# Optimization experiments

Measured on AMD Instinct MI355X. Metric: run time of the kernel, lower is better.

Reference implementation:

```python
import jax, jax.numpy as jnp
import numpy as np

B, T, IN_DIM = 128, 4096, 13
UNITS, MOTOR = 64, 6
LAYERS = [35, 23, 6]   # AutoNCP(64, 6): inter / command / motor neurons
_SPLITS = [35, 58]     # cumulative layer boundaries inside the 64-unit state


def setup_inputs() -> dict:
    keys = iter(jax.random.split(jax.random.key(0), 64))
    def rn(shape, s=0.1):
        return jax.random.normal(next(keys), shape, dtype=jnp.float32) * s
    inp = {"x": jax.random.normal(next(keys), (B, T, IN_DIM), dtype=jnp.float32)}
    # mixed-memory LSTM cell (ncps: input_map has bias, recurrent_map does not)
    inp["lstm_wi"] = rn((4 * UNITS, IN_DIM))
    inp["lstm_wh"] = rn((4 * UNITS, UNITS))
    inp["lstm_b"] = rn((4 * UNITS,))
    # wired CfC layers: ff1/ff2/time_a/time_b acting on concat([input, h])
    in_dims = [IN_DIM] + LAYERS[:-1]
    for i, (d, h) in enumerate(zip(in_dims, LAYERS)):
        for nm in ("w1", "w2", "wa", "wb"):
            inp[f"cfc{i}_{nm}"] = rn((h, d + h))
        for nm in ("b1", "b2", "ba", "bb"):
            inp[f"cfc{i}_{nm}"] = rn((h,))
    inp["gyro_w1"] = rn((32, MOTOR)); inp["gyro_b1"] = rn((32,))
    inp["gyro_w2"] = rn((3, 32));     inp["gyro_b2"] = rn((3,))
    inp["acc_w1"] = rn((32, MOTOR));  inp["acc_b1"] = rn((32,))
    inp["acc_w2"] = rn((3, 32));      inp["acc_b2"] = rn((3,))
    inp["unc_w1"] = rn((16, MOTOR));  inp["unc_b1"] = rn((16,))
    inp["unc_w2"] = rn((6, 16));      inp["unc_b2"] = rn((6,))
    return inp


def _cfc_step(inp, h, p):
    """ncps CfCCell, mode='default', no backbone, ts = 1.0."""
    W1, b1, W2, b2, Wa, ba, Wb, bb = p
    z = jnp.concatenate([inp, h], axis=-1)            # (B, in+hid)
    ff1 = jnp.tanh(z @ W1.T + b1)
    ff2 = jnp.tanh(z @ W2.T + b2)
    t = jax.nn.sigmoid((z @ Wa.T + ba) + (z @ Wb.T + bb))  # t_a*ts + t_b, ts==1
    return ff1 * (1.0 - t) + t * ff2


def reference(x, lstm_wi, lstm_wh, lstm_b,
              cfc0_w1, cfc0_b1, cfc0_w2, cfc0_b2, cfc0_wa, cfc0_ba, cfc0_wb, cfc0_bb,
              cfc1_w1, cfc1_b1, cfc1_w2, cfc1_b2, cfc1_wa, cfc1_ba, cfc1_wb, cfc1_bb,
              cfc2_w1, cfc2_b1, cfc2_w2, cfc2_b2, cfc2_wa, cfc2_ba, cfc2_wb, cfc2_bb,
              gyro_w1, gyro_b1, gyro_w2, gyro_b2,
              acc_w1, acc_b1, acc_w2, acc_b2,
              unc_w1, unc_b1, unc_w2, unc_b2):
    layer_params = (
        (cfc0_w1, cfc0_b1, cfc0_w2, cfc0_b2, cfc0_wa, cfc0_ba, cfc0_wb, cfc0_bb),
        (cfc1_w1, cfc1_b1, cfc1_w2, cfc1_b2, cfc1_wa, cfc1_ba, cfc1_wb, cfc1_bb),
        (cfc2_w1, cfc2_b1, cfc2_w2, cfc2_b2, cfc2_wa, cfc2_ba, cfc2_wb, cfc2_bb),
    )

    def step(carry, xt):  # xt: (B, 13)
        h, c = carry
        # mixed-memory LSTM over the full 64-unit state (forget gate +1.0)
        zg = xt @ lstm_wi.T + lstm_b + h @ lstm_wh.T
        ia, ig, fg, og = jnp.split(zg, 4, axis=-1)
        c_new = c * jax.nn.sigmoid(fg + 1.0) + jnp.tanh(ia) * jax.nn.sigmoid(ig)
        h_lstm = jnp.tanh(c_new) * jax.nn.sigmoid(og)
        # wired CfC: inter -> command -> motor, each fed previous layer's output
        hs = jnp.split(h_lstm, _SPLITS, axis=-1)
        inp = xt
        new_hs = []
        for hi, p in zip(hs, layer_params):
            inp = _cfc_step(inp, hi, p)
            new_hs.append(inp)
        return (jnp.concatenate(new_hs, axis=-1), c_new), inp  # motor out (B,6)

    Bsz = x.shape[0]
    h0 = jnp.zeros((Bsz, UNITS), x.dtype)
    c0 = jnp.zeros((Bsz, UNITS), x.dtype)
    _, outs = jax.lax.scan(step, (h0, c0), jnp.swapaxes(x, 0, 1))
    cfc_out = jnp.swapaxes(outs, 0, 1)  # (B, T, 6)

    gyro = jnp.tanh(cfc_out @ gyro_w1.T + gyro_b1) @ gyro_w2.T + gyro_b2
    acc = jnp.tanh(cfc_out @ acc_w1.T + acc_b1) @ acc_w2.T + acc_b2
    pred = jnp.concatenate([gyro, acc], axis=-1)                      # (B, T, 6)
    unc = jax.nn.softplus(
        jax.nn.relu(cfc_out @ unc_w1.T + unc_b1) @ unc_w2.T + unc_b2)  # (B, T, 6)
    return pred, unc
```

## Files before the change

### kernel.cpp

```cpp
#include <hip/hip_runtime.h>
#include <math.h>

#define BATCH 128
#define TSTEPS 4096
#define INDIM 13
#define XT 64


__device__ __forceinline__ float fsig(float x) {
    return __builtin_amdgcn_rcpf(1.f + __expf(-x));
}
__device__ __forceinline__ float ftanh(float x) {
    float s = fsig(x + x);
    return s + s - 1.f;
}
__device__ __forceinline__ float fsoftplus(float x) {
    return (x > 15.f) ? x : __logf(1.f + __expf(x));
}

__device__ __forceinline__ float qxor1(float v) {
    return __int_as_float(__builtin_amdgcn_update_dpp(
        0, __float_as_int(v), 0xB1, 0xF, 0xF, true));
}
__device__ __forceinline__ float qxor2(float v) {
    return __int_as_float(__builtin_amdgcn_update_dpp(
        0, __float_as_int(v), 0x4E, 0xF, 0xF, true));
}
#define BFLY4(a) { a += qxor1(a); a += qxor2(a); }

#define FMA4(acc, W, q, zv) { acc += zv.x * W##_##q##_0; acc += zv.y * W##_##q##_1; \
                              acc += zv.z * W##_##q##_2; acc += zv.w * W##_##q##_3; }

__global__ __launch_bounds__(256, 1)
void rnn_kernel(const float* __restrict__ x,
                const float* __restrict__ lstm_wi, const float* __restrict__ lstm_wh,
                const float* __restrict__ lstm_b,
                const float* __restrict__ c0w1, const float* __restrict__ c0w2,
                const float* __restrict__ c0wa, const float* __restrict__ c0wb,
                const float* __restrict__ c0b1, const float* __restrict__ c0b2,
                const float* __restrict__ c0ba, const float* __restrict__ c0bb,
                const float* __restrict__ c1w1, const float* __restrict__ c1w2,
                const float* __restrict__ c1wa, const float* __restrict__ c1wb,
                const float* __restrict__ c1b1, const float* __restrict__ c1b2,
                const float* __restrict__ c1ba, const float* __restrict__ c1bb,
                const float* __restrict__ c2w1, const float* __restrict__ c2w2,
                const float* __restrict__ c2wa, const float* __restrict__ c2wb,
                const float* __restrict__ c2b1, const float* __restrict__ c2b2,
                const float* __restrict__ c2ba, const float* __restrict__ c2bb,
                float* __restrict__ out)
{
    const int bb = blockIdx.x;
    const int t  = threadIdx.x;
    const int k  = t & 3;
    const int u  = t >> 2;

    __shared__ __align__(16) float smem[2688];
    float* zL  = smem;
    float* z0  = smem + 96;
    float* z1  = smem + 160;
    float* z2  = smem + 224;
    float* xt0 = smem + 256;
    float* xt1 = smem + 1088;
    float* ot0 = smem + 1920;
    float* ot1 = smem + 2304;

    const long xbase = (long)bb * TSTEPS * INDIM;
    const long obase = (long)bb * TSTEPS * 6;

    auto lwf = [&](int A, int c) -> float {
        int r = A * 64 + u;
        return (c < 13) ? lstm_wi[r * 13 + c]
             : (c < 77) ? lstm_wh[r * 64 + (c - 13)] : 0.f;
    };
#define DEF_WL(A,q) \
    float wl##A##_##q##_0 = lwf(A, 24*k + 4*q + 0); \
    float wl##A##_##q##_1 = lwf(A, 24*k + 4*q + 1); \
    float wl##A##_##q##_2 = lwf(A, 24*k + 4*q + 2); \
    float wl##A##_##q##_3 = lwf(A, 24*k + 4*q + 3);
    DEF_WL(0,0) DEF_WL(0,1) DEF_WL(0,2) DEF_WL(0,3) DEF_WL(0,4) DEF_WL(0,5)
    DEF_WL(1,0) DEF_WL(1,1) DEF_WL(1,2) DEF_WL(1,3) DEF_WL(1,4) DEF_WL(1,5)
    DEF_WL(2,0) DEF_WL(2,1) DEF_WL(2,2) DEF_WL(2,3) DEF_WL(2,4) DEF_WL(2,5)
    DEF_WL(3,0) DEF_WL(3,1) DEF_WL(3,2) DEF_WL(3,3) DEF_WL(3,4) DEF_WL(3,5)
#undef DEF_WL
    const float bL0 = lstm_b[u];
    const float bL1 = lstm_b[64 + u];
    const float bL2 = lstm_b[128 + u];
    const float bL3 = lstm_b[192 + u];

    const int grp  = (u < 35) ? 0 : (u < 58) ? 1 : 2;
    const int row  = (grp == 0) ? u : (grp == 1) ? (u - 35) : (u - 58);
    const int rl   = (grp == 0) ? 48 : (grp == 1) ? 58 : 29;
    const int clen = (grp == 0) ? 12 : (grp == 1) ? 16 : 8;
    const int cb   = clen * k;
    const float *W0p, *W1p, *W2p, *W3p;
    float bC0, bC1, bC2, bC3;
    if (grp == 0) {
        W0p = c0w1 + row * 48; W1p = c0w2 + row * 48;
        W2p = c0wa + row * 48; W3p = c0wb + row * 48;
        bC0 = c0b1[row]; bC1 = c0b2[row]; bC2 = c0ba[row]; bC3 = c0bb[row];
    } else if (grp == 1) {
        W0p = c1w1 + row * 58; W1p = c1w2 + row * 58;
        W2p = c1wa + row * 58; W3p = c1wb + row * 58;
        bC0 = c1b1[row]; bC1 = c1b2[row]; bC2 = c1ba[row]; bC3 = c1bb[row];
    } else {
        W0p = c2w1 + row * 29; W1p = c2w2 + row * 29;
        W2p = c2wa + row * 29; W3p = c2wb + row * 29;
        bC0 = c2b1[row]; bC1 = c2b2[row]; bC2 = c2ba[row]; bC3 = c2bb[row];
    }
    auto cwf = [&](const float* W, int c) -> float {
        int cc = cb + c;
        return (c < clen && cc < rl) ? W[cc] : 0.f;
    };
#define DEF_WC(A,q) \
    float wc##A##_##q##_0 = cwf(W##A##p, 4*q + 0); \
    float wc##A##_##q##_1 = cwf(W##A##p, 4*q + 1); \
    float wc##A##_##q##_2 = cwf(W##A##p, 4*q + 2); \
    float wc##A##_##q##_3 = cwf(W##A##p, 4*q + 3);
    DEF_WC(0,0) DEF_WC(0,1) DEF_WC(0,2) DEF_WC(0,3)
    DEF_WC(1,0) DEF_WC(1,1) DEF_WC(1,2) DEF_WC(1,3)
    DEF_WC(2,0) DEF_WC(2,1) DEF_WC(2,2) DEF_WC(2,3)
    DEF_WC(3,0) DEF_WC(3,1) DEF_WC(3,2) DEF_WC(3,3)
#undef DEF_WC

    float creg = 0.f;

    smem[t] = 0.f;
    if (t < 208) {
        float4 xi = *(const float4*)(x + xbase + 4 * t);
        *(float4*)&xt0[4 * t] = xi;
    }
    if (t < 13) { float x0 = x[xbase + t]; zL[t] = x0; z0[t] = x0; }
    __syncthreads();

    #pragma unroll 1
    for (int ts = 0; ts < TSTEPS; ++ts) {
        const int par = (ts >> 6) & 1;
        const int lts = ts & 63;

        {
            const float4* zc = (const float4*)(zL + 24 * k);
            float4 q0 = zc[0], q1 = zc[1], q2 = zc[2],
                   q3 = zc[3], q4 = zc[4], q5 = zc[5];
            float a0 = 0.f, a1 = 0.f, a2 = 0.f, a3 = 0.f;
            FMA4(a0, wl0, 0, q0) FMA4(a0, wl0, 1, q1) FMA4(a0, wl0, 2, q2)
            FMA4(a0, wl0, 3, q3) FMA4(a0, wl0, 4, q4) FMA4(a0, wl0, 5, q5)
            FMA4(a1, wl1, 0, q0) FMA4(a1, wl1, 1, q1) FMA4(a1, wl1, 2, q2)
            FMA4(a1, wl1, 3, q3) FMA4(a1, wl1, 4, q4) FMA4(a1, wl1, 5, q5)
            FMA4(a2, wl2, 0, q0) FMA4(a2, wl2, 1, q1) FMA4(a2, wl2, 2, q2)
            FMA4(a2, wl2, 3, q3) FMA4(a2, wl2, 4, q4) FMA4(a2, wl2, 5, q5)
            FMA4(a3, wl3, 0, q0) FMA4(a3, wl3, 1, q1) FMA4(a3, wl3, 2, q2)
            FMA4(a3, wl3, 3, q3) FMA4(a3, wl3, 4, q4) FMA4(a3, wl3, 5, q5)
            BFLY4(a0) BFLY4(a1) BFLY4(a2) BFLY4(a3)
            a0 += bL0; a1 += bL1; a2 += bL2; a3 += bL3;
            float cn = creg * fsig(a2 + 1.f) + ftanh(a0) * fsig(a1);
            creg = cn;
            float hl = ftanh(cn) * fsig(a3);
            if (k == 0) {
                if (u < 35)      z0[13 + u] = hl;
                else if (u < 58) z1[u]      = hl;
                else             z2[u - 35] = hl;
            }
        }
        __syncthreads();

        if (grp == 0) {
            const float4* zc = (const float4*)(z0 + 12 * k);
            float4 v0 = zc[0], v1 = zc[1], v2 = zc[2];
            float a0 = 0.f, a1 = 0.f, a2 = 0.f, a3 = 0.f;
            FMA4(a0, wc0, 0, v0) FMA4(a0, wc0, 1, v1) FMA4(a0, wc0, 2, v2)
            FMA4(a1, wc1, 0, v0) FMA4(a1, wc1, 1, v1) FMA4(a1, wc1, 2, v2)
            FMA4(a2, wc2, 0, v0) FMA4(a2, wc2, 1, v1) FMA4(a2, wc2, 2, v2)
            FMA4(a3, wc3, 0, v0) FMA4(a3, wc3, 1, v1) FMA4(a3, wc3, 2, v2)
            BFLY4(a0) BFLY4(a1) BFLY4(a2) BFLY4(a3)
            a0 += bC0; a1 += bC1; a2 += bC2; a3 += bC3;
            float tg = fsig(a2 + a3);
            float f1 = ftanh(a0), f2 = ftanh(a1);
            float o = f1 + tg * (f2 - f1);
            if (k == 0) { z1[row] = o; zL[13 + row] = o; }
        } else {
            if (lts == 62 && (ts + 2) < TSTEPS) {
                int i = (t - 140) * 2;
                float* dst = par ? xt0 : xt1;
                const float* src = x + xbase + (long)(ts + 2) * 13;
                if (i < 208)     *(float4*)&dst[4*i]     = *(const float4*)(src + 4*i);
                if (i + 1 < 208) *(float4*)&dst[4*(i+1)] = *(const float4*)(src + 4*(i+1));
            }
            if (lts == 0 && ts > 0) {
                int i = t - 140;
                if (i < 96) {
                    const float* src = par ? ot0 : ot1;
                    float4 v = *(const float4*)&src[4 * i];
                    *(float4*)(out + obase + (long)(ts - XT) * 6 + 4 * i) = v;
                }
            }
        }
        __syncthreads();

        if (grp == 1) {
            const float4* zc = (const float4*)(z1 + 16 * k);
            float4 v0 = zc[0], v1 = zc[1], v2 = zc[2], v3 = zc[3];
            float a0 = 0.f, a1 = 0.f, a2 = 0.f, a3 = 0.f;
            FMA4(a0, wc0, 0, v0) FMA4(a0, wc0, 1, v1) FMA4(a0, wc0, 2, v2) FMA4(a0, wc0, 3, v3)
            FMA4(a1, wc1, 0, v0) FMA4(a1, wc1, 1, v1) FMA4(a1, wc1, 2, v2) FMA4(a1, wc1, 3, v3)
            FMA4(a2, wc2, 0, v0) FMA4(a2, wc2, 1, v1) FMA4(a2, wc2, 2, v2) FMA4(a2, wc2, 3, v3)
            FMA4(a3, wc3, 0, v0) FMA4(a3, wc3, 1, v1) FMA4(a3, wc3, 2, v2) FMA4(a3, wc3, 3, v3)
            BFLY4(a0) BFLY4(a1) BFLY4(a2) BFLY4(a3)
            a0 += bC0; a1 += bC1; a2 += bC2; a3 += bC3;
            float tg = fsig(a2 + a3);
            float f1 = ftanh(a0), f2 = ftanh(a1);
            float o = f1 + tg * (f2 - f1);
            if (k == 0) { z2[row] = o; zL[48 + row] = o; }
        }
        __syncthreads();

        if (grp == 2) {
            const float4* zc = (const float4*)(z2 + 8 * k);
            float4 v0 = zc[0], v1 = zc[1];
            float a0 = 0.f, a1 = 0.f, a2 = 0.f, a3 = 0.f;
            FMA4(a0, wc0, 0, v0) FMA4(a0, wc0, 1, v1)
            FMA4(a1, wc1, 0, v0) FMA4(a1, wc1, 1, v1)
            FMA4(a2, wc2, 0, v0) FMA4(a2, wc2, 1, v1)
            FMA4(a3, wc3, 0, v0) FMA4(a3, wc3, 1, v1)
            BFLY4(a0) BFLY4(a1) BFLY4(a2) BFLY4(a3)
            a0 += bC0; a1 += bC1; a2 += bC2; a3 += bC3;
            float tg = fsig(a2 + a3);
            float f1 = ftanh(a0), f2 = ftanh(a1);
            float o = f1 + tg * (f2 - f1);
            if (k == 0) {
                zL[71 + row] = o;
                float* ob = par ? ot1 : ot0;
                ob[lts * 6 + row] = o;
            }
        } else if (t < 13 && (ts + 1) < TSTEPS) {
            const float* xb = (((ts + 1) >> 6) & 1) ? xt1 : xt0;
            float xn = xb[((ts + 1) & 63) * 13 + t];
            zL[t] = xn; z0[t] = xn;
        }
        __syncthreads();
    }

    if (t < 96) {
        float4 v = *(const float4*)&ot1[4 * t];
        *(float4*)(out + obase + (long)(TSTEPS - XT) * 6 + 4 * t) = v;
    }
}

#define S_GW1 0
#define S_GB1 192
#define S_GW2 224
#define S_GB2 320
#define S_AW1 323
#define S_AB1 515
#define S_AW2 547
#define S_AB2 643
#define S_UW1 646
#define S_UB1 742
#define S_UW2 758
#define S_UB2 854
#define S_TOT 860

__global__ __launch_bounds__(256)
void head_kernel(const float* __restrict__ gw1, const float* __restrict__ gb1,
                 const float* __restrict__ gw2, const float* __restrict__ gb2,
                 const float* __restrict__ aw1, const float* __restrict__ ab1,
                 const float* __restrict__ aw2, const float* __restrict__ ab2,
                 const float* __restrict__ uw1, const float* __restrict__ ub1,
                 const float* __restrict__ uw2, const float* __restrict__ ub2,
                 float* __restrict__ out)
{
    __shared__ float s[S_TOT];
    const int t = threadIdx.x;
    if (t < 192) { s[S_GW1 + t] = gw1[t]; s[S_AW1 + t] = aw1[t]; }
    if (t < 96)  { s[S_GW2 + t] = gw2[t]; s[S_AW2 + t] = aw2[t];
                   s[S_UW1 + t] = uw1[t]; s[S_UW2 + t] = uw2[t]; }
    if (t < 32)  { s[S_GB1 + t] = gb1[t]; s[S_AB1 + t] = ab1[t]; }
    if (t < 16)  { s[S_UB1 + t] = ub1[t]; }
    if (t < 3)   { s[S_GB2 + t] = gb2[t]; s[S_AB2 + t] = ab2[t]; }
    if (t < 6)   { s[S_UB2 + t] = ub2[t]; }
    __syncthreads();

    const long p = (long)blockIdx.x * 256 + t;
    const long base = p * 6;
    float m0 = out[base+0], m1 = out[base+1], m2 = out[base+2];
    float m3 = out[base+3], m4 = out[base+4], m5 = out[base+5];

    float gy0 = s[S_GB2+0], gy1 = s[S_GB2+1], gy2 = s[S_GB2+2];
    float ac0 = s[S_AB2+0], ac1 = s[S_AB2+1], ac2 = s[S_AB2+2];
    #pragma unroll
    for (int i = 0; i < 32; ++i) {
        float hg = s[S_GB1+i] + s[S_GW1+i*6+0]*m0 + s[S_GW1+i*6+1]*m1
                 + s[S_GW1+i*6+2]*m2 + s[S_GW1+i*6+3]*m3
                 + s[S_GW1+i*6+4]*m4 + s[S_GW1+i*6+5]*m5;
        hg = ftanh(hg);
// ... 80 lines not shown
```

Baseline: 5.327 ms.

## Restructure recurrent step into two barriers with per-wave redundant CfC layers

Reorganizes each timestep so the command and motor CfC layers are computed redundantly inside every wavefront, using wave-local LDS copies and an lgkmcnt fence in place of block-wide barriers, then fuses them with the next LSTM step. The inter layer and the input staging run in a first phase. State buffers are double-buffered by timestep parity, and the loop gains a prologue iteration. This cuts the per-step __syncthreads from four to two, which shortens the serial critical path. The cost is extra redundant compute, more registers for the duplicated weights, and reliance on the LDS fence giving correct intra-wave ordering.

```diff
diff --git a/kernel.cpp b/kernel.cpp
--- a/kernel.cpp
+++ b/kernel.cpp
@@ -30,6 +30,9 @@
 
 #define FMA4(acc, W, q, zv) { acc += zv.x * W##_##q##_0; acc += zv.y * W##_##q##_1; \
                               acc += zv.z * W##_##q##_2; acc += zv.w * W##_##q##_3; }
+
+#define LDS_FENCE() { asm volatile("s_waitcnt lgkmcnt(0)" ::: "memory"); \
+                      __builtin_amdgcn_sched_barrier(0); }
 
 __global__ __launch_bounds__(256, 1)
 void rnn_kernel(const float* __restrict__ x,
@@ -53,16 +56,22 @@
     const int t  = threadIdx.x;
     const int k  = t & 3;
     const int u  = t >> 2;
-
-    __shared__ __align__(16) float smem[2688];
-    float* zL  = smem;
-    float* z0  = smem + 96;
-    float* z1  = smem + 160;
-    float* z2  = smem + 224;
-    float* xt0 = smem + 256;
-    float* xt1 = smem + 1088;
-    float* ot0 = smem + 1920;
-    float* ot1 = smem + 2304;
+    const int l  = t & 63;
+    const int w  = t >> 6;
+    const int cu1 = l >> 1, h1 = l & 1;
+    const int c2i = l - 46;
+    const int cu2 = c2i >> 1, h2 = c2i & 1;
+
+    __shared__ __align__(16) float smem[3152];
+    float* z0  = smem;
+    float* zLa = smem + 96;
+    float* z1  = smem + 144;
+    float* z2  = smem + 272;
+    float* zLb = smem + 528;
+    float* xt0 = smem + 720;
+    float* xt1 = smem + 1552;
+    float* ot0 = smem + 2384;
+    float* ot1 = smem + 2768;
 
     const long xbase = (long)bb * TSTEPS * INDIM;
     const long obase = (long)bb * TSTEPS * 6;
@@ -87,154 +96,215 @@
     const float bL2 = lstm_b[128 + u];
     const float bL3 = lstm_b[192 + u];
 
-    const int grp  = (u < 35) ? 0 : (u < 58) ? 1 : 2;
-    const int row  = (grp == 0) ? u : (grp == 1) ? (u - 35) : (u - 58);
-    const int rl   = (grp == 0) ? 48 : (grp == 1) ? 58 : 29;
-    const int clen = (grp == 0) ? 12 : (grp == 1) ? 16 : 8;
-    const int cb   = clen * k;
-    const float *W0p, *W1p, *W2p, *W3p;
-    float bC0, bC1, bC2, bC3;
-    if (grp == 0) {
-        W0p = c0w1 + row * 48; W1p = c0w2 + row * 48;
-        W2p = c0wa + row * 48; W3p = c0wb + row * 48;
-        bC0 = c0b1[row]; bC1 = c0b2[row]; bC2 = c0ba[row]; bC3 = c0bb[row];
-    } else if (grp == 1) {
-        W0p = c1w1 + row * 58; W1p = c1w2 + row * 58;
-        W2p = c1wa + row * 58; W3p = c1wb + row * 58;
-        bC0 = c1b1[row]; bC1 = c1b2[row]; bC2 = c1ba[row]; bC3 = c1bb[row];
-    } else {
-        W0p = c2w1 + row * 29; W1p = c2w2 + row * 29;
-        W2p = c2wa + row * 29; W3p = c2wb + row * 29;
-        bC0 = c2b1[row]; bC1 = c2b2[row]; bC2 = c2ba[row]; bC3 = c2bb[row];
-    }
-    auto cwf = [&](const float* W, int c) -> float {
-        int cc = cb + c;
-        return (c < clen && cc < rl) ? W[cc] : 0.f;
+    const float *P0 = c0w1, *P1 = c0w2, *P2 = c0wa, *P3 = c0wb;
+    auto c0f = [&](const float* Wp, int c) -> float {
+        return (t < 140) ? Wp[u * 48 + 12 * k + c] : 0.f;
     };
-#define DEF_WC(A,q) \
-    float wc##A##_##q##_0 = cwf(W##A##p, 4*q + 0); \
-    float wc##A##_##q##_1 = cwf(W##A##p, 4*q + 1); \
-    float wc##A##_##q##_2 = cwf(W##A##p, 4*q + 2); \
-    float wc##A##_##q##_3 = cwf(W##A##p, 4*q + 3);
-    DEF_WC(0,0) DEF_WC(0,1) DEF_WC(0,2) DEF_WC(0,3)
-    DEF_WC(1,0) DEF_WC(1,1) DEF_WC(1,2) DEF_WC(1,3)
-    DEF_WC(2,0) DEF_WC(2,1) DEF_WC(2,2) DEF_WC(2,3)
-    DEF_WC(3,0) DEF_WC(3,1) DEF_WC(3,2) DEF_WC(3,3)
-#undef DEF_WC
+#define DEF_WA(A,q) \
+    float wa##A##_##q##_0 = c0f(P##A, 4*q + 0); \
+    float wa##A##_##q##_1 = c0f(P##A, 4*q + 1); \
+    float wa##A##_##q##_2 = c0f(P##A, 4*q + 2); \
+    float wa##A##_##q##_3 = c0f(P##A, 4*q + 3);
+    DEF_WA(0,0) DEF_WA(0,1) DEF_WA(0,2)
+    DEF_WA(1,0) DEF_WA(1,1) DEF_WA(1,2)
+    DEF_WA(2,0) DEF_WA(2,1) DEF_WA(2,2)
+    DEF_WA(3,0) DEF_WA(3,1) DEF_WA(3,2)
+#undef DEF_WA
+    const float bA0 = (t < 140) ? c0b1[u] : 0.f;
+    const float bA1 = (t < 140) ? c0b2[u] : 0.f;
+    const float bA2 = (t < 140) ? c0ba[u] : 0.f;
+    const float bA3 = (t < 140) ? c0bb[u] : 0.f;
+
+    const float *D0 = c1w1, *D1 = c1w2, *D2 = c1wa, *D3 = c1wb;
+    auto c1f = [&](const float* Wp, int c) -> float {
+        const int col = 32 * h1 + c;
+        return (l < 46 && col < 58) ? Wp[cu1 * 58 + col] : 0.f;
+    };
+#define DEF_WD(A,q) \
+    float wd##A##_##q##_0 = c1f(D##A, 4*q + 0); \
+    float wd##A##_##q##_1 = c1f(D##A, 4*q + 1); \
+    float wd##A##_##q##_2 = c1f(D##A, 4*q + 2); \
+    float wd##A##_##q##_3 = c1f(D##A, 4*q + 3);
+    DEF_WD(0,0) DEF_WD(0,1) DEF_WD(0,2) DEF_WD(0,3)
+    DEF_WD(0,4) DEF_WD(0,5) DEF_WD(0,6) DEF_WD(0,7)
+    DEF_WD(1,0) DEF_WD(1,1) DEF_WD(1,2) DEF_WD(1,3)
+    DEF_WD(1,4) DEF_WD(1,5) DEF_WD(1,6) DEF_WD(1,7)
+    DEF_WD(2,0) DEF_WD(2,1) DEF_WD(2,2) DEF_WD(2,3)
+    DEF_WD(2,4) DEF_WD(2,5) DEF_WD(2,6) DEF_WD(2,7)
+    DEF_WD(3,0) DEF_WD(3,1) DEF_WD(3,2) DEF_WD(3,3)
+    DEF_WD(3,4) DEF_WD(3,5) DEF_WD(3,6) DEF_WD(3,7)
+#undef DEF_WD
+    const float bD0 = (l < 46) ? c1b1[cu1] : 0.f;
+    const float bD1 = (l < 46) ? c1b2[cu1] : 0.f;
+    const float bD2 = (l < 46) ? c1ba[cu1] : 0.f;
+    const float bD3 = (l < 46) ? c1bb[cu1] : 0.f;
+
+    const float *E0 = c2w1, *E1 = c2w2, *E2 = c2wa, *E3 = c2wb;
+    auto c2f = [&](const float* Wp, int c) -> float {
+        const int col = 16 * h2 + c;
+        return (c2i >= 0 && c2i < 12 && col < 29) ? Wp[cu2 * 29 + col] : 0.f;
+    };
+#define DEF_WE(A,q) \
+    float we##A##_##q##_0 = c2f(E##A, 4*q + 0); \
+    float we##A##_##q##_1 = c2f(E##A, 4*q + 1); \
+    float we##A##_##q##_2 = c2f(E##A, 4*q + 2); \
+    float we##A##_##q##_3 = c2f(E##A, 4*q + 3);
+    DEF_WE(0,0) DEF_WE(0,1) DEF_WE(0,2) DEF_WE(0,3)
+    DEF_WE(1,0) DEF_WE(1,1) DEF_WE(1,2) DEF_WE(1,3)
+    DEF_WE(2,0) DEF_WE(2,1) DEF_WE(2,2) DEF_WE(2,3)
+    DEF_WE(3,0) DEF_WE(3,1) DEF_WE(3,2) DEF_WE(3,3)
+#undef DEF_WE
+    const float bE0 = (c2i >= 0 && c2i < 12) ? c2b1[cu2] : 0.f;
+    const float bE1 = (c2i >= 0 && c2i < 12) ? c2b2[cu2] : 0.f;
+    const float bE2 = (c2i >= 0 && c2i < 12) ? c2ba[cu2] : 0.f;
+    const float bE3 = (c2i >= 0 && c2i < 12) ? c2bb[cu2] : 0.f;
 
     float creg = 0.f;
 
-    smem[t] = 0.f;
+    for (int i = t; i < 720; i += 256) smem[i] = 0.f;
     if (t < 208) {
         float4 xi = *(const float4*)(x + xbase + 4 * t);
         *(float4*)&xt0[4 * t] = xi;
     }
-    if (t < 13) { float x0 = x[xbase + t]; zL[t] = x0; z0[t] = x0; }
     __syncthreads();
 
     #pragma unroll 1
-    for (int ts = 0; ts < TSTEPS; ++ts) {
-        const int par = (ts >> 6) & 1;
-        const int lts = ts & 63;
-
-        {
-            const float4* zc = (const float4*)(zL + 24 * k);
-            float4 q0 = zc[0], q1 = zc[1], q2 = zc[2],
-                   q3 = zc[3], q4 = zc[4], q5 = zc[5];
-            float a0 = 0.f, a1 = 0.f, a2 = 0.f, a3 = 0.f;
-            FMA4(a0, wl0, 0, q0) FMA4(a0, wl0, 1, q1) FMA4(a0, wl0, 2, q2)
-            FMA4(a0, wl0, 3, q3) FMA4(a0, wl0, 4, q4) FMA4(a0, wl0, 5, q5)
-            FMA4(a1, wl1, 0, q0) FMA4(a1, wl1, 1, q1) FMA4(a1, wl1, 2, q2)
-            FMA4(a1, wl1, 3, q3) FMA4(a1, wl1, 4, q4) FMA4(a1, wl1, 5, q5)
-            FMA4(a2, wl2, 0, q0) FMA4(a2, wl2, 1, q1) FMA4(a2, wl2, 2, q2)
-            FMA4(a2, wl2, 3, q3) FMA4(a2, wl2, 4, q4) FMA4(a2, wl2, 5, q5)
-            FMA4(a3, wl3, 0, q0) FMA4(a3, wl3, 1, q1) FMA4(a3, wl3, 2, q2)
-            FMA4(a3, wl3, 3, q3) FMA4(a3, wl3, 4, q4) FMA4(a3, wl3, 5, q5)
-            BFLY4(a0) BFLY4(a1) BFLY4(a2) BFLY4(a3)
-            a0 += bL0; a1 += bL1; a2 += bL2; a3 += bL3;
-            float cn = creg * fsig(a2 + 1.f) + ftanh(a0) * fsig(a1);
-            creg = cn;
-            float hl = ftanh(cn) * fsig(a3);
-            if (k == 0) {
-                if (u < 35)      z0[13 + u] = hl;
-                else if (u < 58) z1[u]      = hl;
-                else             z2[u - 35] = hl;
-            }
-        }
-        __syncthreads();
-
-        if (grp == 0) {
-            const float4* zc = (const float4*)(z0 + 12 * k);
+    for (int ts = -1; ts < TSTEPS; ++ts) {
+        const int par0 = ts & 1;
+        const int par1 = par0 ^ 1;
+        const int lts  = ts & 63;
+        const int tpar = (ts >> 6) & 1;
+        const bool run = (ts >= 0);
+
+        if (run && t < 140) {
+            const float4* zc = (const float4*)(z0 + 48 * par0 + 12 * k);
             float4 v0 = zc[0], v1 = zc[1], v2 = zc[2];
             float a0 = 0.f, a1 = 0.f, a2 = 0.f, a3 = 0.f;
-            FMA4(a0, wc0, 0, v0) FMA4(a0, wc0, 1, v1) FMA4(a0, wc0, 2, v2)
-            FMA4(a1, wc1, 0, v0) FMA4(a1, wc1, 1, v1) FMA4(a1, wc1, 2, v2)
-            FMA4(a2, wc2, 0, v0) FMA4(a2, wc2, 1, v1) FMA4(a2, wc2, 2, v2)
-            FMA4(a3, wc3, 0, v0) FMA4(a3, wc3, 1, v1) FMA4(a3, wc3, 2, v2)
+            FMA4(a0, wa0, 0, v0) FMA4(a0, wa0, 1, v1) FMA4(a0, wa0, 2, v2)
+            FMA4(a1, wa1, 0, v0) FMA4(a1, wa1, 1, v1) FMA4(a1, wa1, 2, v2)
+            FMA4(a2, wa2, 0, v0) FMA4(a2, wa2, 1, v1) FMA4(a2, wa2, 2, v2)
+            FMA4(a3, wa3, 0, v0) FMA4(a3, wa3, 1, v1) FMA4(a3, wa3, 2, v2)
             BFLY4(a0) BFLY4(a1) BFLY4(a2) BFLY4(a3)
-            a0 += bC0; a1 += bC1; a2 += bC2; a3 += bC3;
+            a0 += bA0; a1 += bA1; a2 += bA2; a3 += bA3;
             float tg = fsig(a2 + a3);
             float f1 = ftanh(a0), f2 = ftanh(a1);
             float o = f1 + tg * (f2 - f1);
-            if (k == 0) { z1[row] = o; zL[13 + row] = o; }
-        } else {
-            if (lts == 62 && (ts + 2) < TSTEPS) {
+            if (k == 0) { zLa[13 + u] = o; z1[64 * par0 + u] = o; }
+        } else if (t >= 140) {
+            if (run && lts == 62 && (ts + 2) < TSTEPS) {
                 int i = (t - 140) * 2;
-                float* dst = par ? xt0 : xt1;
+                float* dst = tpar ? xt0 : xt1;
                 const float* src = x + xbase + (long)(ts + 2) * 13;
                 if (i < 208)     *(float4*)&dst[4*i]     = *(const float4*)(src + 4*i);
                 if (i + 1 < 208) *(float4*)&dst[4*(i+1)] = *(const float4*)(src + 4*(i+1));
             }
-            if (lts == 0 && ts > 0) {
+            if (run && lts == 0 && ts > 0) {
                 int i = t - 140;
                 if (i < 96) {
-                    const float* src = par ? ot0 : ot1;
+                    const float* src = tpar ? ot0 : ot1;
                     float4 v = *(const float4*)&src[4 * i];
                     *(float4*)(out + obase + (long)(ts - XT) * 6 + 4 * i) = v;
                 }
             }
         }
-        __syncthreads();
-
-        if (grp == 1) {
-            const float4* zc = (const float4*)(z1 + 16 * k);
-            float4 v0 = zc[0], v1 = zc[1], v2 = zc[2], v3 = zc[3];
-            float a0 = 0.f, a1 = 0.f, a2 = 0.f, a3 = 0.f;
-            FMA4(a0, wc0, 0, v0) FMA4(a0, wc0, 1, v1) FMA4(a0, wc0, 2, v2) FMA4(a0, wc0, 3, v3)
-            FMA4(a1, wc1, 0, v0) FMA4(a1, wc1, 1, v1) FMA4(a1, wc1, 2, v2) FMA4(a1, wc1, 3, v3)
-            FMA4(a2, wc2, 0, v0) FMA4(a2, wc2, 1, v1) FMA4(a2, wc2, 2, v2) FMA4(a2, wc2, 3, v3)
-            FMA4(a3, wc3, 0, v0) FMA4(a3, wc3, 1, v1) FMA4(a3, wc3, 2, v2) FMA4(a3, wc3, 3, v3)
-            BFLY4(a0) BFLY4(a1) BFLY4(a2) BFLY4(a3)
-            a0 += bC0; a1 += bC1; a2 += bC2; a3 += bC3;
-            float tg = fsig(a2 + a3);
-            float f1 = ftanh(a0), f2 = ftanh(a1);
-            float o = f1 + tg * (f2 - f1);
-            if (k == 0) { z2[row] = o; zL[48 + row] = o; }
+        if (t >= 140 && t < 166 && (ts + 1) < TSTEPS) {
+            const int i = t - 140;
+            const float* xb = (((ts + 1) >> 6) & 1) ? xt1 : xt0;
+            const int c = (i < 13) ? i : (i - 13);
+            const float xn = xb[((ts + 1) & 63) * 13 + c];
+            if (i < 13) zLa[c] = xn;
+            else        z0[48 * par1 + c] = xn;
         }
         __syncthreads();
 
-        if (grp == 2) {
-            const float4* zc = (const float4*)(z2 + 8 * k);
-            float4 v0 = zc[0], v1 = zc[1];
-            float a0 = 0.f, a1 = 0.f, a2 = 0.f, a3 = 0.f;
-            FMA4(a0, wc0, 0, v0) FMA4(a0, wc0, 1, v1)
-            FMA4(a1, wc1, 0, v0) FMA4(a1, wc1, 1, v1)
-            FMA4(a2, wc2, 0, v0) FMA4(a2, wc2, 1, v1)
-            FMA4(a3, wc3, 0, v0) FMA4(a3, wc3, 1, v1)
-            BFLY4(a0) BFLY4(a1) BFLY4(a2) BFLY4(a3)
-            a0 += bC0; a1 += bC1; a2 += bC2; a3 += bC3;
-            float tg = fsig(a2 + a3);
-            float f1 = ftanh(a0), f2 = ftanh(a1);
-            float o = f1 + tg * (f2 - f1);
-            if (k == 0) {
-                zL[71 + row] = o;
-                float* ob = par ? ot1 : ot0;
-                ob[lts * 6 + row] = o;
-            }
-        } else if (t < 13 && (ts + 1) < TSTEPS) {
-            const float* xb = (((ts + 1) >> 6) & 1) ? xt1 : xt0;
-            float xn = xb[((ts + 1) & 63) * 13 + t];
-            zL[t] = xn; z0[t] = xn;
+        {
+            float4 y0, y1, y2, y3, y4, y5, y6, y7;
+            if (l < 46) {
+                const float4* zc = (const float4*)(z1 + 64 * par0 + 32 * h1);
+                y0 = zc[0]; y1 = zc[1]; y2 = zc[2]; y3 = zc[3];
+                y4 = zc[4]; y5 = zc[5]; y6 = zc[6]; y7 = zc[7];
+            }
+            float4 q0, q1, q2, q3, q4, q5;
+            if (k < 2) {
+                const float4* zc = (const float4*)(zLa + 24 * k);
+                q0 = zc[0]; q1 = zc[1]; q2 = zc[2];
+                q3 = zc[3]; q4 = zc[4]; q5 = zc[5];
+            }
+
+            if (run && l < 46) {
+                float a0 = 0.f, a1 = 0.f, a2 = 0.f, a3 = 0.f;
+                FMA4(a0, wd0, 0, y0) FMA4(a0, wd0, 1, y1) FMA4(a0, wd0, 2, y2) FMA4(a0, wd0, 3, y3)
+                FMA4(a0, wd0, 4, y4) FMA4(a0, wd0, 5, y5) FMA4(a0, wd0, 6, y6) FMA4(a0, wd0, 7, y7)
+                FMA4(a1, wd1, 0, y0) FMA4(a1, wd1, 1, y1) FMA4(a1, wd1, 2, y2) FMA4(a1, wd1, 3, y3)
+                FMA4(a1, wd1, 4, y4) FMA4(a1, wd1, 5, y5) FMA4(a1, wd1, 6, y6) FMA4(a1, wd1, 7, y7)
+                FMA4(a2, wd2, 0, y0) FMA4(a2, wd2, 1, y1) FMA4(a2, wd2, 2, y2) FMA4(a2, wd2, 3, y3)
+                FMA4(a2, wd2, 4, y4) FMA4(a2, wd2, 5, y5) FMA4(a2, wd2, 6, y6) FMA4(a2, wd2, 7, y7)
+                FMA4(a3, wd3, 0, y0) FMA4(a3, wd3, 1, y1) FMA4(a3, wd3, 2, y2) FMA4(a3, wd3, 3, y3)
+                FMA4(a3, wd3, 4, y4) FMA4(a3, wd3, 5, y5) FMA4(a3, wd3, 6, y6) FMA4(a3, wd3, 7, y7)
+                a0 += qxor1(a0); a1 += qxor1(a1); a2 += qxor1(a2); a3 += qxor1(a3);
+                a0 += bD0; a1 += bD1; a2 += bD2; a3 += bD3;
+                float tg = fsig(a2 + a3);
+                float f1 = ftanh(a0), f2 = ftanh(a1);
+                float o = f1 + tg * (f2 - f1);
+                if (h1 == 0) {
+                    z2[64 * w + 32 * par0 + cu1] = o;
+                    zLb[48 * w + cu1] = o;
+                }
+            }
+            LDS_FENCE();
+
+            if (run && c2i >= 0 && c2i < 12) {
+                const float4* zc = (const float4*)(z2 + 64 * w + 32 * par0 + 16 * h2);
+                float4 v0 = zc[0], v1 = zc[1], v2 = zc[2], v3 = zc[3];
+                float a0 = 0.f, a1 = 0.f, a2 = 0.f, a3 = 0.f;
+                FMA4(a0, we0, 0, v0) FMA4(a0, we0, 1, v1) FMA4(a0, we0, 2, v2) FMA4(a0, we0, 3, v3)
+                FMA4(a1, we1, 0, v0) FMA4(a1, we1, 1, v1) FMA4(a1, we1, 2, v2) FMA4(a1, we1, 3, v3)
+                FMA4(a2, we2, 0, v0) FMA4(a2, we2, 1, v1) FMA4(a2, we2, 2, v2) FMA4(a2, we2, 3, v3)
+                FMA4(a3, we3, 0, v0) FMA4(a3, we3, 1, v1) FMA4(a3, we3, 2, v2) FMA4(a3, we3, 3, v3)
+                a0 += qxor1(a0); a1 += qxor1(a1); a2 += qxor1(a2); a3 += qxor1(a3);
+                a0 += bE0; a1 += bE1; a2 += bE2; a3 += bE3;
+                float tg = fsig(a2 + a3);
+                float f1 = ftanh(a0), f2 = ftanh(a1);
+                float o = f1 + tg * (f2 - f1);
+                if (h2 == 0) {
+                    zLb[48 * w + 23 + cu2] = o;
+                    if (w == 0) {
+                        float* ob = tpar ? ot1 : ot0;
+                        ob[lts * 6 + cu2] = o;
+                    }
+                }
+            }
+            LDS_FENCE();
+
+            if (k >= 2) {
+                const float4* zc = (const float4*)(zLb + 48 * w + 24 * (k - 2));
+                q0 = zc[0]; q1 = zc[1]; q2 = zc[2];
+                q3 = zc[3]; q4 = zc[4]; q5 = zc[5];
+            }
+            {
+                float a0 = 0.f, a1 = 0.f, a2 = 0.f, a3 = 0.f;
+                FMA4(a0, wl0, 0, q0) FMA4(a0, wl0, 1, q1) FMA4(a0, wl0, 2, q2)
+                FMA4(a0, wl0, 3, q3) FMA4(a0, wl0, 4, q4) FMA4(a0, wl0, 5, q5)
+                FMA4(a1, wl1, 0, q0) FMA4(a1, wl1, 1, q1) FMA4(a1, wl1, 2, q2)
+                FMA4(a1, wl1, 3, q3) FMA4(a1, wl1, 4, q4) FMA4(a1, wl1, 5, q5)
+                FMA4(a2, wl2, 0, q0) FMA4(a2, wl2, 1, q1) FMA4(a2, wl2, 2, q2)
+                FMA4(a2, wl2, 3, q3) FMA4(a2, wl2, 4, q4) FMA4(a2, wl2, 5, q5)
+                FMA4(a3, wl3, 0, q0) FMA4(a3, wl3, 1, q1) FMA4(a3, wl3, 2, q2)
+                FMA4(a3, wl3, 3, q3) FMA4(a3, wl3, 4, q4) FMA4(a3, wl3, 5, q5)
+                BFLY4(a0) BFLY4(a1) BFLY4(a2) BFLY4(a3)
+                a0 += bL0; a1 += bL1; a2 += bL2; a3 += bL3;
+                float cn = creg * fsig(a2 + 1.f) + ftanh(a0) * fsig(a1);
+                creg = cn;
+                float hl = ftanh(cn) * fsig(a3);
+                if (k == 0) {
+                    if (u < 35)      z0[48 * par1 + 13 + u] = hl;
+                    else if (u < 58) z1[64 * par1 + u]      = hl;
+                    else {
+                        const int j = 32 * par1 + 23 + (u - 58);
+                        z2[j] = hl; z2[64 + j] = hl; z2[128 + j] = hl; z2[192 + j] = hl;
+                    }
+                }
+            }
         }
         __syncthreads();
     }
```

Result: slower. 8.246 ms (+54.8%).

## Fold motor CfC layer into next step's LSTM phase, dropping a barrier

Applied to the files above, without the earlier changes.

Each wavefront now redundantly computes the motor-layer CfC (layer 2) for the previous timestep at the start of the LSTM phase. It uses lanes 40-63 with register-held weights and exchanges the result through per-wave LDS with only an lgkmcnt wait instead of a block barrier. The LSTM then adds the motor contribution explicitly. z0 and the motor hidden slice are double-buffered by step parity, and the x load moves into the layer-0 phase. This removes one of four __syncthreads per timestep, at the cost of extra redundant FMAs and register pressure in every wave plus an epilogue to finish the last step.

```diff
diff --git a/kernel.cpp b/kernel.cpp
--- a/kernel.cpp
+++ b/kernel.cpp
@@ -30,6 +30,9 @@
 
 #define FMA4(acc, W, q, zv) { acc += zv.x * W##_##q##_0; acc += zv.y * W##_##q##_1; \
                               acc += zv.z * W##_##q##_2; acc += zv.w * W##_##q##_3; }
+
+#define LDS_FENCE() { asm volatile("s_waitcnt lgkmcnt(0)" ::: "memory"); \
+                      __builtin_amdgcn_sched_barrier(0); }
 
 __global__ __launch_bounds__(256, 1)
 void rnn_kernel(const float* __restrict__ x,
@@ -53,16 +56,19 @@
     const int t  = threadIdx.x;
     const int k  = t & 3;
     const int u  = t >> 2;
-
-    __shared__ __align__(16) float smem[2688];
+    const int l  = t & 63;
+    const int w  = t >> 6;
+
+    __shared__ __align__(16) float smem[2736];
     float* zL  = smem;
     float* z0  = smem + 96;
-    float* z1  = smem + 160;
-    float* z2  = smem + 224;
-    float* xt0 = smem + 256;
-    float* xt1 = smem + 1088;
-    float* ot0 = smem + 1920;
-    float* ot1 = smem + 2304;
+    float* z1  = smem + 192;
+    float* z2h = smem + 256;
+    float* zLw = smem + 272;
+    float* xt0 = smem + 304;
+    float* xt1 = smem + 1136;
+    float* ot0 = smem + 1968;
+    float* ot1 = smem + 2352;
 
     const long xbase = (long)bb * TSTEPS * INDIM;
     const long obase = (long)bb * TSTEPS * 6;
@@ -122,25 +128,61 @@
     DEF_WC(3,0) DEF_WC(3,1) DEF_WC(3,2) DEF_WC(3,3)
 #undef DEF_WC
 
+    const int c2a = (l >= 40) ? 1 : 0;
+    const int c2k = c2a ? ((l - 40) & 3) : 0;
+    const int c2u = c2a ? ((l - 40) >> 2) : 0;
+    auto gwf = [&](const float* W, int j) -> float {
+        int col = (c2k < 3) ? (8 * c2k + j) : (23 + j);
+        int lim = (c2k < 3) ? 23 : 29;
+        return (c2a && col < lim) ? W[c2u * 29 + col] : 0.f;
+    };
+#define DEF_WG(A,q) \
+    float wg##A##_##q##_0 = gwf(G##A, 4*q + 0); \
+    float wg##A##_##q##_1 = gwf(G##A, 4*q + 1); \
+    float wg##A##_##q##_2 = gwf(G##A, 4*q + 2); \
+    float wg##A##_##q##_3 = gwf(G##A, 4*q + 3);
+    const float *G0 = c2w1, *G1 = c2w2, *G2 = c2wa, *G3 = c2wb;
+    DEF_WG(0,0) DEF_WG(0,1)
+    DEF_WG(1,0) DEF_WG(1,1)
+    DEF_WG(2,0) DEF_WG(2,1)
+    DEF_WG(3,0) DEF_WG(3,1)
+#undef DEF_WG
+    const float bE0 = c2a ? c2b1[c2u] : 0.f;
+    const float bE1 = c2a ? c2b2[c2u] : 0.f;
+    const float bE2 = c2a ? c2ba[c2u] : 0.f;
+    const float bE3 = c2a ? c2bb[c2u] : 0.f;
+
     float creg = 0.f;
 
-    smem[t] = 0.f;
+    for (int i = t; i < 304; i += 256) smem[i] = 0.f;
     if (t < 208) {
         float4 xi = *(const float4*)(x + xbase + 4 * t);
         *(float4*)&xt0[4 * t] = xi;
     }
-    if (t < 13) { float x0 = x[xbase + t]; zL[t] = x0; z0[t] = x0; }
+    if (t < 13) { float x0v = x[xbase + t]; zL[t] = x0v; z0[t] = x0v; }
     __syncthreads();
 
     #pragma unroll 1
     for (int ts = 0; ts < TSTEPS; ++ts) {
-        const int par = (ts >> 6) & 1;
-        const int lts = ts & 63;
+        const int par0 = ts & 1;
+        const int par1 = par0 ^ 1;
+        const int lts  = ts & 63;
+        const int tpar = (ts >> 6) & 1;
 
         {
+            const float* cp = (c2k < 3) ? (zL + 48 + 8 * c2k) : (z2h + 8 * par1);
+            float4 cv0 = ((const float4*)cp)[0];
+            float4 cv1 = ((const float4*)cp)[1];
             const float4* zc = (const float4*)(zL + 24 * k);
             float4 q0 = zc[0], q1 = zc[1], q2 = zc[2],
                    q3 = zc[3], q4 = zc[4], q5 = zc[5];
+
+            float g0 = 0.f, g1 = 0.f, g2 = 0.f, g3 = 0.f;
+            FMA4(g0, wg0, 0, cv0) FMA4(g0, wg0, 1, cv1)
+            FMA4(g1, wg1, 0, cv0) FMA4(g1, wg1, 1, cv1)
+            FMA4(g2, wg2, 0, cv0) FMA4(g2, wg2, 1, cv1)
+            FMA4(g3, wg3, 0, cv0) FMA4(g3, wg3, 1, cv1)
+
             float a0 = 0.f, a1 = 0.f, a2 = 0.f, a3 = 0.f;
             FMA4(a0, wl0, 0, q0) FMA4(a0, wl0, 1, q1) FMA4(a0, wl0, 2, q2)
             FMA4(a0, wl0, 3, q3) FMA4(a0, wl0, 4, q4) FMA4(a0, wl0, 5, q5)
@@ -150,21 +192,51 @@
             FMA4(a2, wl2, 3, q3) FMA4(a2, wl2, 4, q4) FMA4(a2, wl2, 5, q5)
             FMA4(a3, wl3, 0, q0) FMA4(a3, wl3, 1, q1) FMA4(a3, wl3, 2, q2)
             FMA4(a3, wl3, 3, q3) FMA4(a3, wl3, 4, q4) FMA4(a3, wl3, 5, q5)
+
+            BFLY4(g0) BFLY4(g1) BFLY4(g2) BFLY4(g3)
+            g0 += bE0; g1 += bE1; g2 += bE2; g3 += bE3;
+            float tg2 = fsig(g2 + g3);
+            float f1g = ftanh(g0), f2g = ftanh(g1);
+            float og  = f1g + tg2 * (f2g - f1g);
+            if (ts > 0 && c2a && ((l - 40) & 3) == 0) {
+                zLw[8 * w + c2u] = og;
+                if (w == 0) {
+                    float* ob = (((ts - 1) >> 6) & 1) ? ot1 : ot0;
+                    ob[((ts - 1) & 63) * 6 + c2u] = og;
+                }
+            }
+            LDS_FENCE();
+
+            float4 oza = *(const float4*)(zLw + 8 * w);
+            float2 ozb = *(const float2*)(zLw + 8 * w + 4);
+            if (k == 2) {
+                a0 += oza.x * wl0_5_3; a1 += oza.x * wl1_5_3;
+                a2 += oza.x * wl2_5_3; a3 += oza.x * wl3_5_3;
+            } else if (k == 3) {
+                a0 += oza.y * wl0_0_0; a0 += oza.z * wl0_0_1; a0 += oza.w * wl0_0_2;
+                a0 += ozb.x * wl0_0_3; a0 += ozb.y * wl0_1_0;
+                a1 += oza.y * wl1_0_0; a1 += oza.z * wl1_0_1; a1 += oza.w * wl1_0_2;
+                a1 += ozb.x * wl1_0_3; a1 += ozb.y * wl1_1_0;
+                a2 += oza.y * wl2_0_0; a2 += oza.z * wl2_0_1; a2 += oza.w * wl2_0_2;
+                a2 += ozb.x * wl2_0_3; a2 += ozb.y * wl2_1_0;
+                a3 += oza.y * wl3_0_0; a3 += oza.z * wl3_0_1; a3 += oza.w * wl3_0_2;
+                a3 += ozb.x * wl3_0_3; a3 += ozb.y * wl3_1_0;
+            }
             BFLY4(a0) BFLY4(a1) BFLY4(a2) BFLY4(a3)
             a0 += bL0; a1 += bL1; a2 += bL2; a3 += bL3;
             float cn = creg * fsig(a2 + 1.f) + ftanh(a0) * fsig(a1);
             creg = cn;
             float hl = ftanh(cn) * fsig(a3);
             if (k == 0) {
-                if (u < 35)      z0[13 + u] = hl;
-                else if (u < 58) z1[u]      = hl;
-                else             z2[u - 35] = hl;
+                if (u < 35)      z0[48 * par0 + 13 + u] = hl;
+                else if (u < 58) z1[u] = hl;
+                else             z2h[8 * par0 + (u - 58)] = hl;
             }
         }
         __syncthreads();
 
-        if (grp == 0) {
-            const float4* zc = (const float4*)(z0 + 12 * k);
+        if (t < 140) {
+            const float4* zc = (const float4*)(z0 + 48 * par0 + 12 * k);
             float4 v0 = zc[0], v1 = zc[1], v2 = zc[2];
             float a0 = 0.f, a1 = 0.f, a2 = 0.f, a3 = 0.f;
             FMA4(a0, wc0, 0, v0) FMA4(a0, wc0, 1, v1) FMA4(a0, wc0, 2, v2)
@@ -180,7 +252,7 @@
         } else {
             if (lts == 62 && (ts + 2) < TSTEPS) {
                 int i = (t - 140) * 2;
-                float* dst = par ? xt0 : xt1;
+                float* dst = tpar ? xt0 : xt1;
                 const float* src = x + xbase + (long)(ts + 2) * 13;
                 if (i < 208)     *(float4*)&dst[4*i]     = *(const float4*)(src + 4*i);
                 if (i + 1 < 208) *(float4*)&dst[4*(i+1)] = *(const float4*)(src + 4*(i+1));
@@ -188,11 +260,17 @@
             if (lts == 0 && ts > 0) {
                 int i = t - 140;
                 if (i < 96) {
-                    const float* src = par ? ot0 : ot1;
+                    const float* src = tpar ? ot0 : ot1;
                     float4 v = *(const float4*)&src[4 * i];
                     *(float4*)(out + obase + (long)(ts - XT) * 6 + 4 * i) = v;
                 }
             }
+        }
+        if (t >= 192 && t < 205 && (ts + 1) < TSTEPS) {
+            const int i = t - 192;
+            const float* xb = (((ts + 1) >> 6) & 1) ? xt1 : xt0;
+            float xn = xb[((ts + 1) & 63) * 13 + i];
+            zL[i] = xn; z0[48 * par1 + i] = xn;
         }
         __syncthreads();
 
@@ -209,36 +287,29 @@
             float tg = fsig(a2 + a3);
             float f1 = ftanh(a0), f2 = ftanh(a1);
             float o = f1 + tg * (f2 - f1);
-            if (k == 0) { z2[row] = o; zL[48 + row] = o; }
+            if (k == 0) { zL[48 + row] = o; }
         }
         __syncthreads();
-
-        if (grp == 2) {
-            const float4* zc = (const float4*)(z2 + 8 * k);
-            float4 v0 = zc[0], v1 = zc[1];
-            float a0 = 0.f, a1 = 0.f, a2 = 0.f, a3 = 0.f;
-            FMA4(a0, wc0, 0, v0) FMA4(a0, wc0, 1, v1)
-            FMA4(a1, wc1, 0, v0) FMA4(a1, wc1, 1, v1)
-            FMA4(a2, wc2, 0, v0) FMA4(a2, wc2, 1, v1)
-            FMA4(a3, wc3, 0, v0) FMA4(a3, wc3, 1, v1)
-            BFLY4(a0) BFLY4(a1) BFLY4(a2) BFLY4(a3)
-            a0 += bC0; a1 += bC1; a2 += bC2; a3 += bC3;
-            float tg = fsig(a2 + a3);
-            float f1 = ftanh(a0), f2 = ftanh(a1);
-            float o = f1 + tg * (f2 - f1);
-            if (k == 0) {
-                zL[71 + row] = o;
-                float* ob = par ? ot1 : ot0;
-                ob[lts * 6 + row] = o;
-            }
-        } else if (t < 13 && (ts + 1) < TSTEPS) {
-            const float* xb = (((ts + 1) >> 6) & 1) ? xt1 : xt0;
-            float xn = xb[((ts + 1) & 63) * 13 + t];
-            zL[t] = xn; z0[t] = xn;
-        }
-        __syncthreads();
-    }
-
+    }
+
+    {
+        const float* cp = (c2k < 3) ? (zL + 48 + 8 * c2k) : (z2h + 8);
+        float4 cv0 = ((const float4*)cp)[0];
+        float4 cv1 = ((const float4*)cp)[1];
+        float g0 = 0.f, g1 = 0.f, g2 = 0.f, g3 = 0.f;
+        FMA4(g0, wg0, 0, cv0) FMA4(g0, wg0, 1, cv1)
+        FMA4(g1, wg1, 0, cv0) FMA4(g1, wg1, 1, cv1)
+        FMA4(g2, wg2, 0, cv0) FMA4(g2, wg2, 1, cv1)
+        FMA4(g3, wg3, 0, cv0) FMA4(g3, wg3, 1, cv1)
+        BFLY4(g0) BFLY4(g1) BFLY4(g2) BFLY4(g3)
+        g0 += bE0; g1 += bE1; g2 += bE2; g3 += bE3;
+        float tg2 = fsig(g2 + g3);
+        float f1g = ftanh(g0), f2g = ftanh(g1);
+        float og  = f1g + tg2 * (f2g - f1g);
+        if (c2a && ((l - 40) & 3) == 0 && w == 0)
+            ot1[63 * 6 + c2u] = og;
+    }
+    __syncthreads();
     if (t < 96) {
         float4 v = *(const float4*)&ot1[4 * t];
         *(float4*)(out + obase + (long)(TSTEPS - XT) * 6 + 4 * t) = v;
```

Result: slower. 5.598 ms (+5.1%).

## Precompute LSTM input and inter-layer gate partials off the critical path

Applied to the files above, without the earlier changes.

Splits the LSTM gate matvec so the contributions from the next input and the inter-neuron state (which become available early) are computed by idle threads during the command-layer phase and stored in shared memory. The critical LSTM phase then reduces only over the command/motor state (8 columns per lane instead of 24), shortening the serial dependency chain per timestep. In exchange it costs large per-thread weight arrays (98 extra registers on 128 threads), extra shared memory, and a reshuffled zL layout, which may hurt occupancy or cause spills.

```diff
diff --git a/kernel.cpp b/kernel.cpp
--- a/kernel.cpp
+++ b/kernel.cpp
@@ -54,38 +54,55 @@
     const int k  = t & 3;
     const int u  = t >> 2;
 
-    __shared__ __align__(16) float smem[2688];
+    __shared__ __align__(16) float smem[2944];
     float* zL  = smem;
     float* z0  = smem + 96;
     float* z1  = smem + 160;
     float* z2  = smem + 224;
-    float* xt0 = smem + 256;
-    float* xt1 = smem + 1088;
-    float* ot0 = smem + 1920;
-    float* ot1 = smem + 2304;
+    float* Pb  = smem + 256;
+    float* xt0 = smem + 512;
+    float* xt1 = smem + 1344;
+    float* ot0 = smem + 2176;
+    float* ot1 = smem + 2560;
 
     const long xbase = (long)bb * TSTEPS * INDIM;
     const long obase = (long)bb * TSTEPS * 6;
 
-    auto lwf = [&](int A, int c) -> float {
-        int r = A * 64 + u;
-        return (c < 13) ? lstm_wi[r * 13 + c]
-             : (c < 77) ? lstm_wh[r * 64 + (c - 13)] : 0.f;
-    };
-#define DEF_WL(A,q) \
-    float wl##A##_##q##_0 = lwf(A, 24*k + 4*q + 0); \
-    float wl##A##_##q##_1 = lwf(A, 24*k + 4*q + 1); \
-    float wl##A##_##q##_2 = lwf(A, 24*k + 4*q + 2); \
-    float wl##A##_##q##_3 = lwf(A, 24*k + 4*q + 3);
-    DEF_WL(0,0) DEF_WL(0,1) DEF_WL(0,2) DEF_WL(0,3) DEF_WL(0,4) DEF_WL(0,5)
-    DEF_WL(1,0) DEF_WL(1,1) DEF_WL(1,2) DEF_WL(1,3) DEF_WL(1,4) DEF_WL(1,5)
-    DEF_WL(2,0) DEF_WL(2,1) DEF_WL(2,2) DEF_WL(2,3) DEF_WL(2,4) DEF_WL(2,5)
-    DEF_WL(3,0) DEF_WL(3,1) DEF_WL(3,2) DEF_WL(3,3) DEF_WL(3,4) DEF_WL(3,5)
-#undef DEF_WL
+    float wl[4][8];
+    #pragma unroll
+    for (int A = 0; A < 4; ++A) {
+        #pragma unroll
+        for (int j = 0; j < 8; ++j) {
+            const int c = 48 + 8 * k + j;
+            const int r = A * 64 + u;
+            float wv = 0.f;
+            if (c <= 70)                 wv = lstm_wh[r * 64 + (c - 13)];
+            else if (c >= 72 && c <= 77) wv = lstm_wh[r * 64 + (c - 14)];
+            wl[A][j] = wv;
+        }
+    }
     const float bL0 = lstm_b[u];
     const float bL1 = lstm_b[64 + u];
     const float bL2 = lstm_b[128 + u];
     const float bL3 = lstm_b[192 + u];
+
+    float wpx0[13], wpx1[13], wpo0[36], wpo1[36];
+    {
+        const int A  = t & 3;
+        const int u0 = (t >> 2) & 31;
+        const int u1 = 32 + u0;
+        const bool pw = (t < 128);
+        #pragma unroll
+        for (int c = 0; c < 13; ++c) {
+            wpx0[c] = pw ? lstm_wi[(A * 64 + u0) * 13 + c] : 0.f;
+            wpx1[c] = pw ? lstm_wi[(A * 64 + u1) * 13 + c] : 0.f;
+        }
+        #pragma unroll
+        for (int c = 0; c < 36; ++c) {
+            wpo0[c] = (pw && c < 35) ? lstm_wh[(A * 64 + u0) * 64 + c] : 0.f;
+            wpo1[c] = (pw && c < 35) ? lstm_wh[(A * 64 + u1) * 64 + c] : 0.f;
+        }
+    }
 
     const int grp  = (u < 35) ? 0 : (u < 58) ? 1 : 2;
     const int row  = (grp == 0) ? u : (grp == 1) ? (u - 35) : (u - 58);
@@ -124,13 +141,37 @@
 
     float creg = 0.f;
 
-    smem[t] = 0.f;
+    for (int i = t; i < 512; i += 256) smem[i] = 0.f;
     if (t < 208) {
         float4 xi = *(const float4*)(x + xbase + 4 * t);
         *(float4*)&xt0[4 * t] = xi;
     }
-    if (t < 13) { float x0 = x[xbase + t]; zL[t] = x0; z0[t] = x0; }
+    if (t < 13) { z0[t] = x[xbase + t]; }
     __syncthreads();
+
+    if (t < 128) {
+        float s0 = 0.f, s1 = 0.f;
+        #pragma unroll
+        for (int c = 0; c < 13; ++c) {
+            float xv = xt0[c];
+            s0 += xv * wpx0[c]; s1 += xv * wpx1[c];
+        }
+        #pragma unroll
+        for (int i = 0; i < 9; ++i) {
+            float4 v = *(const float4*)(z1 + 4 * i);
+            s0 += v.x * wpo0[4*i]   + v.y * wpo0[4*i+1]
+                + v.z * wpo0[4*i+2] + v.w * wpo0[4*i+3];
+            s1 += v.x * wpo1[4*i]   + v.y * wpo1[4*i+1]
+                + v.z * wpo1[4*i+2] + v.w * wpo1[4*i+3];
+        }
+        Pb[t] = s0; Pb[t + 128] = s1;
+    }
+    __syncthreads();
+
+    float4 q0 = *(const float4*)(zL + 48 + 8 * k);
+    float4 q1 = *(const float4*)(zL + 52 + 8 * k);
+    float4 pf = {0.f, 0.f, 0.f, 0.f};
+    if (k == 0) pf = *(const float4*)(Pb + 4 * u);
 
     #pragma unroll 1
     for (int ts = 0; ts < TSTEPS; ++ts) {
@@ -138,18 +179,20 @@
         const int lts = ts & 63;
 
         {
-            const float4* zc = (const float4*)(zL + 24 * k);
-            float4 q0 = zc[0], q1 = zc[1], q2 = zc[2],
-                   q3 = zc[3], q4 = zc[4], q5 = zc[5];
-            float a0 = 0.f, a1 = 0.f, a2 = 0.f, a3 = 0.f;
-            FMA4(a0, wl0, 0, q0) FMA4(a0, wl0, 1, q1) FMA4(a0, wl0, 2, q2)
-            FMA4(a0, wl0, 3, q3) FMA4(a0, wl0, 4, q4) FMA4(a0, wl0, 5, q5)
-            FMA4(a1, wl1, 0, q0) FMA4(a1, wl1, 1, q1) FMA4(a1, wl1, 2, q2)
-            FMA4(a1, wl1, 3, q3) FMA4(a1, wl1, 4, q4) FMA4(a1, wl1, 5, q5)
-            FMA4(a2, wl2, 0, q0) FMA4(a2, wl2, 1, q1) FMA4(a2, wl2, 2, q2)
-            FMA4(a2, wl2, 3, q3) FMA4(a2, wl2, 4, q4) FMA4(a2, wl2, 5, q5)
-            FMA4(a3, wl3, 0, q0) FMA4(a3, wl3, 1, q1) FMA4(a3, wl3, 2, q2)
-            FMA4(a3, wl3, 3, q3) FMA4(a3, wl3, 4, q4) FMA4(a3, wl3, 5, q5)
+            if (k == 3) {
+                q0 = *(const float4*)(zL + 48 + 8 * k);
+                q1 = *(const float4*)(zL + 52 + 8 * k);
+            }
+            float a0 = (k == 0) ? pf.x : 0.f;
+            float a1 = (k == 0) ? pf.y : 0.f;
+            float a2 = (k == 0) ? pf.z : 0.f;
+            float a3 = (k == 0) ? pf.w : 0.f;
+            const float qq[8] = {q0.x, q0.y, q0.z, q0.w, q1.x, q1.y, q1.z, q1.w};
+            #pragma unroll
+            for (int j = 0; j < 8; ++j) {
+                a0 += qq[j] * wl[0][j]; a1 += qq[j] * wl[1][j];
+                a2 += qq[j] * wl[2][j]; a3 += qq[j] * wl[3][j];
+            }
             BFLY4(a0) BFLY4(a1) BFLY4(a2) BFLY4(a3)
             a0 += bL0; a1 += bL1; a2 += bL2; a3 += bL3;
             float cn = creg * fsig(a2 + 1.f) + ftanh(a0) * fsig(a1);
@@ -176,7 +219,7 @@
             float tg = fsig(a2 + a3);
             float f1 = ftanh(a0), f2 = ftanh(a1);
             float o = f1 + tg * (f2 - f1);
-            if (k == 0) { z1[row] = o; zL[13 + row] = o; }
+            if (k == 0) { z1[row] = o; }
         } else {
             if (lts == 62 && (ts + 2) < TSTEPS) {
                 int i = (t - 140) * 2;
@@ -210,9 +253,33 @@
             float f1 = ftanh(a0), f2 = ftanh(a1);
             float o = f1 + tg * (f2 - f1);
             if (k == 0) { z2[row] = o; zL[48 + row] = o; }
+        } else if (t < 128) {
+            const float* xb = (((ts + 1) >> 6) & 1) ? xt1 : xt0;
+            const int xr = ((ts + 1) & 63) * 13;
+            float s0 = 0.f, s1 = 0.f;
+            #pragma unroll
+            for (int c = 0; c < 13; ++c) {
+                float xv = xb[xr + c];
+                s0 += xv * wpx0[c]; s1 += xv * wpx1[c];
+            }
+            #pragma unroll
+            for (int i = 0; i < 9; ++i) {
+                float4 v = *(const float4*)(z1 + 4 * i);
+                s0 += v.x * wpo0[4*i]   + v.y * wpo0[4*i+1]
+                    + v.z * wpo0[4*i+2] + v.w * wpo0[4*i+3];
+                s1 += v.x * wpo1[4*i]   + v.y * wpo1[4*i+1]
+                    + v.z * wpo1[4*i+2] + v.w * wpo1[4*i+3];
+            }
+            Pb[t] = s0; Pb[t + 128] = s1;
+        } else if (t >= 232 && t < 245 && (ts + 1) < TSTEPS) {
+            const float* xb = (((ts + 1) >> 6) & 1) ? xt1 : xt0;
+            z0[t - 232] = xb[((ts + 1) & 63) * 13 + (t - 232)];
         }
         __syncthreads();
 
+        q0 = *(const float4*)(zL + 48 + 8 * k);
+        q1 = *(const float4*)(zL + 52 + 8 * k);
+        if (k == 0) pf = *(const float4*)(Pb + 4 * u);
         if (grp == 2) {
             const float4* zc = (const float4*)(z2 + 8 * k);
             float4 v0 = zc[0], v1 = zc[1];
@@ -227,14 +294,10 @@
             float f1 = ftanh(a0), f2 = ftanh(a1);
             float o = f1 + tg * (f2 - f1);
             if (k == 0) {
-                zL[71 + row] = o;
+                zL[72 + row] = o;
                 float* ob = par ? ot1 : ot0;
                 ob[lts * 6 + row] = o;
             }
-        } else if (t < 13 && (ts + 1) < TSTEPS) {
-            const float* xb = (((ts + 1) >> 6) & 1) ? xt1 : xt0;
-            float xn = xb[((ts + 1) & 63) * 13 + t];
-            zL[t] = xn; z0[t] = xn;
         }
         __syncthreads();
     }
```

Measured after the change: 5.345 ms. Within noise of the previous version (+0.3%).
